# Optimization experiments

Hardware: AMD Instinct MI355X
Metric: run time of the kernel (lower is better)

Reference implementation:

```python
import jax, jax.numpy as jnp
import numpy as np
import math

T = 120      # frame_num == audio_len == max_seq_len
D = 64       # hidden_layer_size
H = 2        # n_head
DH = D // H
DFF = 2 * D
DOUT = 31
PERIOD = 10
EPS = 1e-5
NEG = -1e9
SCALE = 1.0 / math.sqrt(DH)
SLOPES = (1.0 / 16.0, 1.0 / 256.0)  # ALiBi slopes for n_head=2


def _pe():
    # PeriodicPositionalEncoding: sinusoid over one period, tiled
    pos = jnp.arange(PERIOD, dtype=jnp.float32)[:, None]
    div = jnp.exp(jnp.arange(0, D, 2, dtype=jnp.float32) * (-math.log(10000.0) / D))
    s, c = jnp.sin(pos * div), jnp.cos(pos * div)
    pe = jnp.stack([s, c], axis=-1).reshape(PERIOD, D)  # interleave sin/cos
    return jnp.tile(pe, (T // PERIOD + 1, 1))[:T]


def _alibi_mask():
    # causal mask + ALiBi bias: alibi[i,j] = -slope * floor((i-j)/period) for j<=i
    slopes = jnp.array(SLOPES, dtype=jnp.float32)
    i = jnp.arange(T)[:, None]
    j = jnp.arange(T)[None, :]
    rel = ((i - j) // PERIOD).astype(jnp.float32)
    return jnp.where(j <= i, -slopes[:, None, None] * rel, NEG)  # [H,T,T]


def _ln(x, g, b):
    m = x.mean(-1, keepdims=True)
    v = ((x - m) ** 2).mean(-1, keepdims=True)
    return (x - m) / jnp.sqrt(v + EPS) * g + b


def setup_inputs() -> dict:
    key = jax.random.key(0)
    ks = iter(jax.random.split(key, 32))
    n = lambda shape, s=0.05: jax.random.normal(next(ks), shape, dtype=jnp.float32) * s
    inp = {
        'audio': jax.random.normal(next(ks), (1, T, 1024), dtype=jnp.float32),
        'W_audio': n((D, 1024)), 'b_audio': n((D,)),
        'obj_W': n((D, 5)),
        'Wq': n((D, D)), 'bq': n((D,)), 'Wk': n((D, D)), 'bk': n((D,)),
        'Wv': n((D, D)), 'bv': n((D,)), 'Wo': n((D, D)), 'bo': n((D,)),
        'Wv2': n((D, D)), 'bv2': n((D,)), 'Wo2': n((D, D)), 'bo2': n((D,)),
        'g1': jnp.ones((D,)), 'be1': jnp.zeros((D,)),
        'g2': jnp.ones((D,)), 'be2': jnp.zeros((D,)),
        'g3': jnp.ones((D,)), 'be3': jnp.zeros((D,)),
        'W1': n((DFF, D)), 'c1': n((DFF,)), 'W2': n((D, DFF)), 'c2': n((D,)),
        'Wr': n((DOUT, D)), 'br': n((DOUT,)), 'Wm': n((D, DOUT)), 'bm': n((D,)),
    }
    return inp


def _forward(audio, W_audio, b_audio, obj_W, Wq, bq, Wk, bk, Wv, bv, Wo, bo,
             Wv2, bv2, Wo2, bo2, g1, be1, g2, be2, g3, be3,
             W1, c1, W2, c2, Wr, br, Wm, bm):
    mem = audio[0] @ W_audio.T + b_audio          # [S,D], S == T
    style = obj_W[:, 0]                            # obj_vector @ [1,0,0,0,0]
    pe = _pe()
    mask = _alibi_mask()
    slopes = jnp.array(SLOPES, dtype=jnp.float32)
    jarr = jnp.arange(T)

    # enc_dec_mask leaves exactly one memory key per target row (anti-diagonal
    # from the end); the feedback row t at step t always attends memory[-1],
    # so its cross-attn output is just the projected value of the last frame.
    cross_last = (mem[-1] @ Wv2.T + bv2) @ Wo2.T + bo2  # [D]

    def step(emb, t):
        # decode only the last row (row t) of the growing sequence; 1-layer
        # post-norm decoder => row t depends only on input rows 0..t.
        x = emb + pe                                 # PPE over prefix
        xq = jnp.take(x, t, axis=0)                  # [D]
        q = (xq @ Wq.T + bq).reshape(H, DH)
        k = (x @ Wk.T + bk).reshape(T, H, DH)
        v = (x @ Wv.T + bv).reshape(T, H, DH)
        bias = jnp.where(jarr <= t,
                         -slopes[:, None] * ((t - jarr) // PERIOD).astype(jnp.float32),
                         NEG)                        # [H,T]
        sc = jnp.einsum('hd,shd->hs', q, k) * SCALE + bias
        a = jax.nn.softmax(sc, axis=-1)
        sa = jnp.einsum('hs,shd->hd', a, v).reshape(D) @ Wo.T + bo
        h1 = _ln(xq + sa, g1, be1)
        h2 = _ln(h1 + cross_last, g2, be2)
        h3 = _ln(h2 + jax.nn.relu(h2 @ W1.T + c1) @ W2.T + c2, g3, be3)
        new = (h3 @ Wr.T + br) @ Wm.T + bm + style   # vertice_map(vertice_map_r(.)) + style
        emb = jax.lax.dynamic_update_slice(emb, new[None, :], (t + 1, 0))
        return emb, None

    emb0 = jnp.zeros((T, D), audio.dtype).at[0].set(style)
    emb, _ = jax.lax.scan(step, emb0, jnp.arange(T - 1))

    # final full-length decode (last loop iteration of the torch module)
    x = emb + pe
    q = (x @ Wq.T + bq).reshape(T, H, DH)
    k = (x @ Wk.T + bk).reshape(T, H, DH)
    v = (x @ Wv.T + bv).reshape(T, H, DH)
    sc = jnp.einsum('thd,shd->hts', q, k) * SCALE + mask
    a = jax.nn.softmax(sc, axis=-1)
    sa = jnp.einsum('hts,shd->thd', a, v).reshape(T, D) @ Wo.T + bo
    h1 = _ln(x + sa, g1, be1)
    # at length T with S == T the enc_dec_mask aligns target row j <-> memory row j
    cross = (mem @ Wv2.T + bv2) @ Wo2.T + bo2
    h2 = _ln(h1 + cross, g2, be2)
    h3 = _ln(h2 + jax.nn.relu(h2 @ W1.T + c1) @ W2.T + c2, g3, be3)
    return (h3 @ Wr.T + br)[None]                    # [1,T,31]


def reference(audio, W_audio, b_audio, obj_W, Wq, bq, Wk, bk, Wv, bv, Wo, bo,
              Wv2, bv2, Wo2, bo2, g1, be1, g2, be2, g3, be3,
              W1, c1, W2, c2, Wr, br, Wm, bm):
    return _forward(audio, W_audio, b_audio, obj_W, Wq, bq, Wk, bk, Wv, bv, Wo, bo,
                    Wv2, bv2, Wo2, bo2, g1, be1, g2, be2, g3, be3,
                    W1, c1, W2, c2, Wr, br, Wm, bm)
```

## Files before the change

kernel.cpp:

```cpp
#include <hip/hip_runtime.h>

typedef unsigned short u16;
typedef unsigned int   u32;
typedef _Float16 f16;
typedef f16 h2 __attribute__((ext_vector_type(2)));
typedef f16 h4 __attribute__((ext_vector_type(4)));
typedef f16 h8 __attribute__((ext_vector_type(8)));

#define T_    120
#define D_    64
#define DOUT_ 31
#define KROW_ 68
#define VROW_ 132

#if defined(__has_builtin)
#if __has_builtin(__builtin_amdgcn_fdot2)
#define DOT2(a,b,c) __builtin_amdgcn_fdot2((a),(b),(c),false)
#endif
#endif
#ifndef DOT2
#define DOT2(a,b,c) ((float)(a).x*(float)(b).x + ((float)(a).y*(float)(b).y + (c)))
#endif
#define SHV(x,i,j) __builtin_shufflevector((x),(x),(i),(j))

__device__ __forceinline__ h2 pk(float a, float b){
#if defined(__has_builtin) && __has_builtin(__builtin_amdgcn_cvt_pkrtz)
  return __builtin_bit_cast(h2, __builtin_amdgcn_cvt_pkrtz(a, b));
#else
  h2 r; r.x = (f16)a; r.y = (f16)b; return r;
#endif
}
__device__ __forceinline__ float b2f(u16 u){ return __uint_as_float(((u32)u) << 16); }
__device__ __forceinline__ float2 bp2(u32 u){
  float2 r; r.x = __uint_as_float(u << 16); r.y = __uint_as_float(u & 0xffff0000u); return r;
}
__device__ __forceinline__ u16 f2bu(float f){
  u32 u = __float_as_uint(f);
  u32 r = u + 0x7fffu + ((u >> 16) & 1u);
  return (u16)(r >> 16);
}
__device__ __forceinline__ u16 f2h16(float x){
  f16 v = (f16)x; u16 r; __builtin_memcpy(&r, &v, 2); return r;
}
__device__ __forceinline__ float fast_rcp(float x){
#if defined(__has_builtin) && __has_builtin(__builtin_amdgcn_rcpf)
  return __builtin_amdgcn_rcpf(x);
#else
  return 1.f / x;
#endif
}
#define WSYNC() do{ __asm__ __volatile__("" ::: "memory"); __builtin_amdgcn_wave_barrier(); }while(0)

__device__ __forceinline__ float dpp_sum(float x){
  int t;
  t = __builtin_amdgcn_update_dpp(0, __float_as_int(x), 0x111, 0xf, 0xf, true); x += __int_as_float(t);
  t = __builtin_amdgcn_update_dpp(0, __float_as_int(x), 0x112, 0xf, 0xf, true); x += __int_as_float(t);
  t = __builtin_amdgcn_update_dpp(0, __float_as_int(x), 0x114, 0xf, 0xf, true); x += __int_as_float(t);
  t = __builtin_amdgcn_update_dpp(0, __float_as_int(x), 0x118, 0xf, 0xf, true); x += __int_as_float(t);
  t = __builtin_amdgcn_update_dpp(0, __float_as_int(x), 0x142, 0xf, 0xf, true); x += __int_as_float(t);
  t = __builtin_amdgcn_update_dpp(0, __float_as_int(x), 0x143, 0xf, 0xf, true); x += __int_as_float(t);
  return __int_as_float(__builtin_amdgcn_readlane(__float_as_int(x), 63));
}
__device__ __forceinline__ float dpp_max_pos(float x){
  int t;
  t = __builtin_amdgcn_update_dpp(0, __float_as_int(x), 0x111, 0xf, 0xf, true); x = fmaxf(x, __int_as_float(t));
  t = __builtin_amdgcn_update_dpp(0, __float_as_int(x), 0x112, 0xf, 0xf, true); x = fmaxf(x, __int_as_float(t));
  t = __builtin_amdgcn_update_dpp(0, __float_as_int(x), 0x114, 0xf, 0xf, true); x = fmaxf(x, __int_as_float(t));
  t = __builtin_amdgcn_update_dpp(0, __float_as_int(x), 0x118, 0xf, 0xf, true); x = fmaxf(x, __int_as_float(t));
  t = __builtin_amdgcn_update_dpp(0, __float_as_int(x), 0x142, 0xf, 0xf, true); x = fmaxf(x, __int_as_float(t));
  t = __builtin_amdgcn_update_dpp(0, __float_as_int(x), 0x143, 0xf, 0xf, true); x = fmaxf(x, __int_as_float(t));
  return __int_as_float(__builtin_amdgcn_readlane(__float_as_int(x), 63));
}
__device__ __forceinline__ float pe_val(int row, int i){
  const float coef = -0.28782313662425574f;
  int p = row % 10;
  float dv  = __expf((float)(i >> 1) * coef);
  float ang = (float)p * dv;
  return (i & 1) ? __cosf(ang) : __sinf(ang);
}
__device__ __forceinline__ void loadrow32(h2* dst, const float* row){
  #pragma unroll
  for (int r = 0; r < 16; ++r){
    float4 f = ((const float4*)row)[r];
    dst[2*r]   = pk(f.x, f.y);
    dst[2*r+1] = pk(f.z, f.w);
  }
}

__global__ __launch_bounds__(256) void k_pre(const float* __restrict__ audio,
                                             const float* __restrict__ Wa, const float* __restrict__ ba,
                                             const float* __restrict__ Wv2, const float* __restrict__ bv2,
                                             const float* __restrict__ Wo2, const float* __restrict__ bo2,
                                             const float* __restrict__ Wo, const float* __restrict__ W1,
                                             const float* __restrict__ W2, const float* __restrict__ Wr,
                                             const float* __restrict__ Wm, const float* __restrict__ br,
                                             const float* __restrict__ bm,
                                             float* __restrict__ cross, float* __restrict__ Ms,
                                             float* __restrict__ bMv,
                                             u16* __restrict__ wob, u16* __restrict__ w1b,
                                             u16* __restrict__ w2b, u16* __restrict__ wrb){
  const int b = blockIdx.x, tid = threadIdx.x;
  if (b == 120){
    for (int i = tid; i < 4096; i += 256) wob[i] = f2bu(Wo[i]);
    for (int i = tid; i < 8192; i += 256){ w1b[i] = f2bu(W1[i]); w2b[i] = f2bu(W2[i]); }
    for (int i = tid; i < 1984; i += 256) wrb[i] = f2bu(Wr[i]);
    for (int idx = tid; idx < 4096; idx += 256){
      int d = idx >> 6, e = idx & 63;
      float acc = 0.f;
      #pragma unroll
      for (int j = 0; j < 31; ++j) acc += Wm[d*31 + j] * Wr[j*64 + e];
      Ms[idx] = acc;
    }
    if (tid < 64){
      float acc = bm[tid];
      #pragma unroll
      for (int j = 0; j < 31; ++j) acc += Wm[tid*31 + j] * br[j];
      bMv[tid] = acc;
    }
    return;
  }
  __shared__ float ash[1024];
  __shared__ float msh[64], tsh[64];
  for (int i = tid; i < 1024; i += 256) ash[i] = audio[b*1024 + i];
  __syncthreads();
  const int w = tid >> 6, lane = tid & 63;
  for (int d = w*16; d < w*16 + 16; ++d){
    const float4* row = (const float4*)(Wa + d*1024);
    float acc = 0.f;
    #pragma unroll
    for (int m = 0; m < 4; ++m){
      float4 wp = row[lane + 64*m];
      int j = 4*(lane + 64*m);
      acc += wp.x*ash[j] + wp.y*ash[j+1] + wp.z*ash[j+2] + wp.w*ash[j+3];
    }
    acc = dpp_sum(acc);
    if (lane == 0) msh[d] = acc + ba[d];
  }
  __syncthreads();
  if (tid < 64){
    const float4* r1 = (const float4*)(Wv2 + tid*64);
    float a = bv2[tid];
    #pragma unroll
    for (int j = 0; j < 16; ++j){ float4 p = r1[j]; a += p.x*msh[4*j] + p.y*msh[4*j+1] + p.z*msh[4*j+2] + p.w*msh[4*j+3]; }
    tsh[tid] = a;
  }
  __syncthreads();
  if (tid < 64){
    const float4* r2 = (const float4*)(Wo2 + tid*64);
    float c = bo2[tid];
    #pragma unroll
    for (int j = 0; j < 16; ++j){ float4 p = r2[j]; c += p.x*tsh[4*j] + p.y*tsh[4*j+1] + p.z*tsh[4*j+2] + p.w*tsh[4*j+3]; }
    cross[b*64 + tid] = c;
  }
}

__global__ __launch_bounds__(128, 1) void k_scan(
    const float* __restrict__ objW,
    const float* __restrict__ Wq, const float* __restrict__ bq,
    const float* __restrict__ Wk, const float* __restrict__ bk,
    const float* __restrict__ Wv, const float* __restrict__ bv,
    const float* __restrict__ Wo, const float* __restrict__ bo,
    const float* __restrict__ g1, const float* __restrict__ be1,
    const float* __restrict__ g2, const float* __restrict__ be2,
    const float* __restrict__ g3, const float* __restrict__ be3,
    const float* __restrict__ W1, const float* __restrict__ c1,
    const float* __restrict__ W2, const float* __restrict__ c2,
    const float* __restrict__ Ms, const float* __restrict__ bMv,
    const float* __restrict__ cross,
    u16* __restrict__ xw16, u16* __restrict__ Kw16, u16* __restrict__ Vw16)
{
  __shared__ __align__(16) f16 KcS[128*KROW_];
  __shared__ __align__(16) f16 VcS[D_*VROW_];
  __shared__ __align__(16) f16 xwS[T_*D_];
  __shared__ __align__(16) f16 sch[256];
  __shared__ __align__(16) f16 xh[64], qh[64], h2h[64], h3h[64];
  __shared__ __align__(16) f16 at0h[64], at1h[64];
  __shared__ __align__(16) f16 fsh[128];
  __shared__ float h2f[64], xf[64];
  __shared__ float invSh;
  __shared__ float pe_tab[640];

  const int tid = threadIdx.x;
  const int i = tid & 63;
  const bool w0 = tid < 64;

  h2 A[32], B[32], C[32], D[32], E[32];
  float biasA=0.f, biasB=0.f, bo_r=0.f, c1r=0.f, c2_r=0.f, cls_r=0.f;
  float g1r=0.f,b1r=0.f,g2r=0.f,b2r=0.f;
  float mg_r=0.f, u_r=0.f;

  if (w0){
    loadrow32(A, Wq + i*64);
    loadrow32(B, Wv + i*64);
    loadrow32(C, Wo + i*64);
    loadrow32(D, W1 + i*64);
    biasA = bq[i]; biasB = bv[i]; bo_r = bo[i]; c1r = c1[i];
    g1r = g1[i]; b1r = be1[i]; g2r = g2[i]; b2r = be2[i];
    cls_r = cross[119*64 + i];
  } else {
    loadrow32(A, Wk + i*64);
    loadrow32(B, W1 + (64+i)*64);
    loadrow32(C, W2 + i*128);
    loadrow32(D, W2 + i*128 + 64);
    {
      const float4* mr  = (const float4*)(Ms + i*64);
      const float4* gv  = (const float4*)g3;
      const float4* b3v = (const float4*)be3;
      float mg = 0.f, mb = 0.f;
      #pragma unroll
      for (int r = 0; r < 16; ++r){
        float4 f = mr[r], g = gv[r], b = b3v[r];
        float e0 = f.x*g.x, e1 = f.y*g.y, e2 = f.z*g.z, e3 = f.w*g.w;
        E[2*r]   = pk(e0, e1);
        E[2*r+1] = pk(e2, e3);
        mg += (e0+e1)+(e2+e3);
        mb += f.x*b.x + f.y*b.y + f.z*b.z + f.w*b.w;
      }
      mg_r = mg;
      u_r  = bMv[i] + objW[i*5] + mb;
    }
    biasA = bk[i]; c1r = c1[64+i]; c2_r = c2[i];
  }
  { u32* p = (u32*)KcS; for (int idx = tid; idx < 128*KROW_/2; idx += 128) p[idx] = 0; }
  { u32* p = (u32*)VcS; for (int idx = tid; idx < D_*VROW_/2;  idx += 128) p[idx] = 0; }
  for (int idx = tid; idx < 640; idx += 128) pe_tab[idx] = pe_val(idx >> 6, idx & 63);
  if (w0){
    float st = objW[i*5];
    float x0 = st + pe_val(0, i);
    xf[i] = x0; xh[i] = (f16)x0; xwS[i] = (f16)x0;
  }
  __syncthreads();

  int pp = 1;
  for (int t = 0; t < T_-1; ++t){
    float e0r, e1r, inv0v;
    h8 xr[8];
    {
      const h8* xv = (const h8*)xh;
      #pragma unroll
      for (int r = 0; r < 8; ++r) xr[r] = xv[r];
      float a0=biasA,a1=0.f,a2=0.f,a3=0.f;
      #pragma unroll
      for (int r = 0; r < 8; ++r){
        h8 x = xr[r];
        a0 = DOT2(A[4*r+0], SHV(x,0,1), a0);
        a1 = DOT2(A[4*r+1], SHV(x,2,3), a1);
        a2 = DOT2(A[4*r+2], SHV(x,4,5), a2);
        a3 = DOT2(A[4*r+3], SHV(x,6,7), a3);
      }
      float qk = (a0+a1)+(a2+a3);
      if (w0) qh[i] = (f16)qk; else KcS[t*KROW_ + i] = (f16)qk;
    }
    __syncthreads();
    {
      if (w0){
        float v0=biasB,v1=0.f,v2=0.f,v3=0.f;
        #pragma unroll
        for (int r = 0; r < 8; ++r){
          h8 x = xr[r];
          v0 = DOT2(B[4*r+0], SHV(x,0,1), v0); v1 = DOT2(B[4*r+1], SHV(x,2,3), v1);
          v2 = DOT2(B[4*r+2], SHV(x,4,5), v2); v3 = DOT2(B[4*r+3], SHV(x,6,7), v3);
        }
        VcS[i*VROW_ + t] = (f16)((v0+v1)+(v2+v3));
      }
      const int h = tid >> 6, j = i;
      const h8* qv = (const h8*)(qh + h*32);
      const h4* k0 = (const h4*)(KcS + j*KROW_ + h*32);
      const h4* k1 = (const h4*)(KcS + (j+64)*KROW_ + h*32);
      float d0a=0.f,d0b=0.f,d1a=0.f,d1b=0.f;
      #pragma unroll
      for (int r = 0; r < 4; ++r){
        h8 q = qv[r];
        h4 ka = k0[2*r], kb = k0[2*r+1], kc = k1[2*r], kd = k1[2*r+1];
        d0a = DOT2(SHV(ka,0,1), SHV(q,0,1), d0a);
        d0b = DOT2(SHV(ka,2,3), SHV(q,2,3), d0b);
        d0a = DOT2(SHV(kb,0,1), SHV(q,4,5), d0a);
        d0b = DOT2(SHV(kb,2,3), SHV(q,6,7), d0b);
        d1a = DOT2(SHV(kc,0,1), SHV(q,0,1), d1a);
        d1b = DOT2(SHV(kc,2,3), SHV(q,2,3), d1b);
        d1a = DOT2(SHV(kd,0,1), SHV(q,4,5), d1a);
        d1b = DOT2(SHV(kd,2,3), SHV(q,6,7), d1b);
      }
      float d0 = d0a + d0b, d1 = d1a + d1b;
      const float slope = h ? 0.00390625f : 0.0625f;
      int r0 = (t - j) / 10, r1 = (t - j - 64) / 10;
      float s0 = d0*0.17677669529663687f - slope*(float)r0;
      float s1 = d1*0.17677669529663687f - slope*(float)r1;
      e0r = (j      <= t) ? __expf(fminf(s0, 8.f)) : 0.f;
      e1r = (j + 64 <= t) ? __expf(fminf(s1, 8.f)) : 0.f;
      sch[h*128 + j]      = (f16)e0r;
      sch[h*128 + j + 64] = (f16)e1r;
    }
    __syncthreads();
    {
      float den = dpp_sum(e0r + e1r);
      float inv = fast_rcp(den);
      inv0v = inv;
      if (tid == 64) invSh = inv;
      if (w0 || t >= 64){
        const int hd = i >> 5;
        const h8* av = (const h8*)(sch + hd*128) + (w0 ? 0 : 8);
        const h4* vv = (const h4*)(VcS + i*VROW_) + (w0 ? 0 : 16);
        float p0=0.f,p1=0.f,p2=0.f,p3=0.f;
        #pragma unroll
        for (int r = 0; r < 8; ++r){
          h8 a = av[r];
          h4 va = vv[2*r], vb = vv[2*r+1];
          p0 = DOT2(SHV(va,0,1), SHV(a,0,1), p0);
          p1 = DOT2(SHV(va,2,3), SHV(a,2,3), p1);
          p2 = DOT2(SHV(vb,0,1), SHV(a,4,5), p2);
          p3 = DOT2(SHV(vb,2,3), SHV(a,6,7), p3);
        }
        float p = (p0+p1)+(p2+p3);
        if (w0) at0h[i] = (f16)p; else at1h[i] = (f16)p;
      }
    }
    __syncthreads();
    if (w0){
      float inv1v = invSh;
      float xfv = xf[i];
      float l0=0.f,l1=0.f,hh0=0.f,hh1=0.f;
      {
        const h8* a0v = (const h8*)at0h;
        #pragma unroll
        for (int r = 0; r < 4; ++r){
          h8 x = a0v[r];
          l0 = DOT2(C[4*r+0], SHV(x,0,1), l0); l1 = DOT2(C[4*r+1], SHV(x,2,3), l1);
          l0 = DOT2(C[4*r+2], SHV(x,4,5), l0); l1 = DOT2(C[4*r+3], SHV(x,6,7), l1);
        }
        #pragma unroll
        for (int r = 4; r < 8; ++r){
          h8 x = a0v[r];
          hh0 = DOT2(C[4*r+0], SHV(x,0,1), hh0); hh1 = DOT2(C[4*r+1], SHV(x,2,3), hh1);
          hh0 = DOT2(C[4*r+2], SHV(x,4,5), hh0); hh1 = DOT2(C[4*r+3], SHV(x,6,7), hh1);
        }
      }
      if (t >= 64){
        const h8* a1v = (const h8*)at1h;
        #pragma unroll
        for (int r = 0; r < 4; ++r){
          h8 x = a1v[r];
          l0 = DOT2(C[4*r+0], SHV(x,0,1), l0); l1 = DOT2(C[4*r+1], SHV(x,2,3), l1);
          l0 = DOT2(C[4*r+2], SHV(x,4,5), l0); l1 = DOT2(C[4*r+3], SHV(x,6,7), l1);
        }
        #pragma unroll
        for (int r = 4; r < 8; ++r){
          h8 x = a1v[r];
          hh0 = DOT2(C[4*r+0], SHV(x,0,1), hh0); hh1 = DOT2(C[4*r+1], SHV(x,2,3), hh1);
          hh0 = DOT2(C[4*r+2], SHV(x,4,5), hh0); hh1 = DOT2(C[4*r+3], SHV(x,6,7), hh1);
        }
      }
      float sa = bo_r + inv0v*(l0+l1) + inv1v*(hh0+hh1);
      float y = xfv + sa;
      float s = dpp_sum(y), s2 = dpp_sum(y*y);
      float m = s*(1.f/64.f), var = fmaxf(s2*(1.f/64.f) - m*m, 0.f);
      float h1 = (y - m)*rsqrtf(var + 1e-5f)*g1r + b1r;
      float z = h1 + cls_r;
      float sz = dpp_sum(z), sz2 = dpp_sum(z*z);
      float mz = sz*(1.f/64.f), vz = fmaxf(sz2*(1.f/64.f) - mz*mz, 0.f);
      float h2v = (z - mz)*rsqrtf(vz + 1e-5f)*g2r + b2r;
      h2h[i] = (f16)h2v;
      h2f[i] = h2v;
    }
    __syncthreads();
    {
      const h8* hv = (const h8*)h2h;
      float a0=c1r, a1=0.f, a2=0.f, a3=0.f;
      if (w0){
        #pragma unroll
        for (int r = 0; r < 8; ++r){
          h8 x = hv[r];
          a0 = DOT2(D[4*r+0], SHV(x,0,1), a0);
          a1 = DOT2(D[4*r+1], SHV(x,2,3), a1);
          a2 = DOT2(D[4*r+2], SHV(x,4,5), a2);
          a3 = DOT2(D[4*r+3], SHV(x,6,7), a3);
        }
      } else {
        #pragma unroll
        for (int r = 0; r < 8; ++r){
          h8 x = hv[r];
          a0 = DOT2(B[4*r+0], SHV(x,0,1), a0);
          a1 = DOT2(B[4*r+1], SHV(x,2,3), a1);
          a2 = DOT2(B[4*r+2], SHV(x,4,5), a2);
          a3 = DOT2(B[4*r+3], SHV(x,6,7), a3);
        }
      }
      fsh[tid] = (f16)fmaxf((a0+a1)+(a2+a3), 0.f);
    }
    __syncthreads();
    if (!w0){
      float pe_c  = pe_tab[pp*64 + i];
      float h2v_s = h2f[i];
      const h8* fv = (const h8*)fsh;
      float a0=c2_r, a1=0.f, a2=0.f, a3=0.f;
      #pragma unroll
      for (int r = 0; r < 8; ++r){
        h8 x = fv[r];
        a0 = DOT2(C[4*r+0], SHV(x,0,1), a0);
        a1 = DOT2(C[4*r+1], SHV(x,2,3), a1);
        a2 = DOT2(C[4*r+2], SHV(x,4,5), a2);
        a3 = DOT2(C[4*r+3], SHV(x,6,7), a3);
      }
      #pragma unroll
      for (int r = 0; r < 8; ++r){
        h8 x = fv[8+r];
        a0 = DOT2(D[4*r+0], SHV(x,0,1), a0);
        a1 = DOT2(D[4*r+1], SHV(x,2,3), a1);
        a2 = DOT2(D[4*r+2], SHV(x,4,5), a2);
        a3 = DOT2(D[4*r+3], SHV(x,6,7), a3);
      }
      float y3 = h2v_s + (a0+a1)+(a2+a3);
      h3h[i] = (f16)y3;
      WSYNC();
      const h8* hv3 = (const h8*)h3h;
      h8 yr[8];
      #pragma unroll
      for (int r = 0; r < 8; ++r) yr[r] = hv3[r];
      float s = dpp_sum(y3), s2 = dpp_sum(y3*y3);
      float m = s*(1.f/64.f), var = fmaxf(s2*(1.f/64.f) - m*m, 0.f);
      float invs = rsqrtf(var + 1e-5f);
      float m0=0.f, m1=0.f, m2=0.f, m3=0.f;
      #pragma unroll
      for (int r = 0; r < 8; ++r){
        h8 x = yr[r];
        m0 = DOT2(E[4*r+0], SHV(x,0,1), m0);
        m1 = DOT2(E[4*r+1], SHV(x,2,3), m1);
        m2 = DOT2(E[4*r+2], SHV(x,4,5), m2);
        m3 = DOT2(E[4*r+3], SHV(x,6,7), m3);
      }
      float xn = ((m0+m1)+(m2+m3))*invs + (u_r - m*invs*mg_r) + pe_c;
      xf[i] = xn;
      xh[i] = (f16)xn;
      xwS[(t+1)*64 + i] = (f16)xn;
    }
    __syncthreads();
    pp = (pp == 9) ? 0 : pp + 1;
  }
  {
    const h8* xv = (const h8*)xh;
    if (w0){
      float v0=biasB,v1=0.f,v2=0.f,v3=0.f;
      #pragma unroll
      for (int r = 0; r < 8; ++r){
        h8 x = xv[r];
        v0 = DOT2(B[4*r+0], SHV(x,0,1), v0);
        v1 = DOT2(B[4*r+1], SHV(x,2,3), v1);
        v2 = DOT2(B[4*r+2], SHV(x,4,5), v2);
        v3 = DOT2(B[4*r+3], SHV(x,6,7), v3);
      }
      Vw16[119*64 + i] = f2h16((v0+v1)+(v2+v3));
    } else {
      float k0=biasA,k1=0.f,k2=0.f,k3=0.f;
      #pragma unroll
      for (int r = 0; r < 8; ++r){
        h8 x = xv[r];
        k0 = DOT2(A[4*r+0], SHV(x,0,1), k0);
        k1 = DOT2(A[4*r+1], SHV(x,2,3), k1);
        k2 = DOT2(A[4*r+2], SHV(x,4,5), k2);
        k3 = DOT2(A[4*r+3], SHV(x,6,7), k3);
      }
      Kw16[119*64 + i] = f2h16((k0+k1)+(k2+k3));
    }
  }
  {
    const u16* kc = (const u16*)KcS;
    const u16* vc = (const u16*)VcS;
    for (int idx = tid; idx < 119*64; idx += 128){
      int t_ = idx >> 6, d = idx & 63;
      Kw16[idx] = kc[t_*KROW_ + d];
      Vw16[idx] = vc[d*VROW_ + t_];
    }
    const u32* xs32 = (const u32*)xwS;
    for (int idx = tid; idx < T_*D_/2; idx += 128) ((u32*)xw16)[idx] = xs32[idx];
  }
}

__global__ __launch_bounds__(128) void k_final(
    const float* __restrict__ Wq, const float* __restrict__ bq, const float* __restrict__ bo,
    const float* __restrict__ g1, const float* __restrict__ be1,
    const float* __restrict__ g2, const float* __restrict__ be2,
    const float* __restrict__ g3, const float* __restrict__ be3,
    const float* __restrict__ c1, const float* __restrict__ c2, const float* __restrict__ br,
    const u16* __restrict__ wo_b, const u16* __restrict__ w1_b,
    const u16* __restrict__ w2_b, const u16* __restrict__ wr_b,
    const float* __restrict__ cross, const u16* __restrict__ xw16,
    const u16* __restrict__ Kw16, const u16* __restrict__ Vw16,
    float* __restrict__ out)
{
  __shared__ float xs[64], qs[64], at[64], h2s[64], h3s[64], fs[128], sc[256];
  const int irow = blockIdx.x, tid = threadIdx.x;
  const f16* xp = (const f16*)xw16;
  const f16* kp = (const f16*)Kw16;
  const f16* vp = (const f16*)Vw16;
  if (tid < 64) xs[tid] = (float)xp[irow*64 + tid];
  __syncthreads();
  if (tid < 64){
    const float4* wr_ = (const float4*)(Wq + tid*64);
    float acc = bq[tid];
    #pragma unroll
    for (int j = 0; j < 16; ++j){ float4 w = wr_[j]; acc += w.x*xs[4*j] + w.y*xs[4*j+1] + w.z*xs[4*j+2] + w.w*xs[4*j+3]; }
    qs[tid] = acc;
  }
  __syncthreads();
  {
    const int h = tid >> 6, j = tid & 63;
    const float* qh_ = qs + h*32;
    float d0 = 0.f, d1 = 0.f;
    const h4* k0 = (const h4*)(kp + j*64 + h*32);
    #pragma unroll
    for (int w = 0; w < 8; ++w){
      h4 p = k0[w];
      d0 += (float)p.x*qh_[4*w] + (float)p.y*qh_[4*w+1] + (float)p.z*qh_[4*w+2] + (float)p.w*qh_[4*w+3];
    }
    if (j < 56){
      const h4* k1 = (const h4*)(kp + (j+64)*64 + h*32);
      #pragma unroll
      for (int w = 0; w < 8; ++w){
        h4 p = k1[w];
        d1 += (float)p.x*qh_[4*w] + (float)p.y*qh_[4*w+1] + (float)p.z*qh_[4*w+2] + (float)p.w*qh_[4*w+3];
      }
    }
    const float slope = h ? 0.00390625f : 0.0625f;
    float s0 = (j      <= irow) ? d0*0.17677669529663687f - slope*(float)((irow-j)/10)    : -1e30f;
    float s1 = (j + 64 <= irow) ? d1*0.17677669529663687f - slope*(float)((irow-j-64)/10) : -1e30f;
    float m = dpp_max_pos(fmaxf(s0, s1) + 16384.f) - 16384.f;
    float e0 = (j      <= irow) ? __expf(s0 - m) : 0.f;
    float e1 = (j + 64 <= irow) ? __expf(s1 - m) : 0.f;
    float inv = 1.f / dpp_sum(e0 + e1);
    sc[h*128 + j]      = e0*inv;
    sc[h*128 + j + 64] = e1*inv;
  }
  __syncthreads();
  if (tid < 64){
    const float* a = sc + (tid >> 5)*128;
    float a0=0.f,a1=0.f,a2=0.f,a3=0.f;
    #pragma unroll
    for (int jj = 0; jj < 30; ++jj){
      a0 += a[4*jj]   * (float)vp[(4*jj)*64   + tid];
      a1 += a[4*jj+1] * (float)vp[(4*jj+1)*64 + tid];
      a2 += a[4*jj+2] * (float)vp[(4*jj+2)*64 + tid];
      a3 += a[4*jj+3] * (float)vp[(4*jj+3)*64 + tid];
    }
    at[tid] = (a0+a1)+(a2+a3);
  }
  __syncthreads();
  if (tid < 64){
    const u32* orow = (const u32*)(wo_b + tid*64);
    float acc = bo[tid];
    #pragma unroll
    for (int w = 0; w < 32; ++w){ float2 p = bp2(orow[w]); acc += p.x*at[2*w] + p.y*at[2*w+1]; }
    float y = xs[tid] + acc;
    float s = dpp_sum(y), s2 = dpp_sum(y*y);
    float m = s*(1.f/64.f), var = fmaxf(s2*(1.f/64.f) - m*m, 0.f);
    float h1 = (y - m)*rsqrtf(var + 1e-5f)*g1[tid] + be1[tid];
    float z = h1 + cross[irow*64 + tid];
    float sz = dpp_sum(z), sz2 = dpp_sum(z*z);
    float mz = sz*(1.f/64.f), vz = fmaxf(sz2*(1.f/64.f) - mz*mz, 0.f);
    h2s[tid] = (z - mz)*rsqrtf(vz + 1e-5f)*g2[tid] + be2[tid];
  }
  __syncthreads();
  {
    const u32* w1r = (const u32*)(w1_b + tid*64);
    float acc = c1[tid];
    #pragma unroll
    for (int w = 0; w < 32; ++w){ float2 p = bp2(w1r[w]); acc += p.x*h2s[2*w] + p.y*h2s[2*w+1]; }
    fs[tid] = fmaxf(acc, 0.f);
  }
  __syncthreads();
  if (tid < 64){
    const u32* w2r = (const u32*)(w2_b + tid*128);
    float acc = c2[tid];
    #pragma unroll
    for (int w = 0; w < 64; ++w){ float2 p = bp2(w2r[w]); acc += p.x*fs[2*w] + p.y*fs[2*w+1]; }
    float y = h2s[tid] + acc;
    float s = dpp_sum(y), s2 = dpp_sum(y*y);
    float m = s*(1.f/64.f), var = fmaxf(s2*(1.f/64.f) - m*m, 0.f);
    h3s[tid] = (y - m)*rsqrtf(var + 1e-5f)*g3[tid] + be3[tid];
  }
  __syncthreads();
  if (tid < DOUT_){
    const u32* rr = (const u32*)(wr_b + tid*64);
    float acc = br[tid];
    #pragma unroll
    for (int w = 0; w < 32; ++w){ float2 p = bp2(rr[w]); acc += p.x*h3s[2*w] + p.y*h3s[2*w+1]; }
    out[irow*DOUT_ + tid] = acc;
  }
}

extern "C" void kernel_launch(void* const* d_in, const int* in_sizes, int n_in,
                              void* d_out, int out_size, void* d_ws, size_t ws_size,
                              hipStream_t stream){
  const float* audio=(const float*)d_in[0];
  const float* Wa   =(const float*)d_in[1];
  const float* ba   =(const float*)d_in[2];
  const float* objW =(const float*)d_in[3];
  const float* Wq   =(const float*)d_in[4];
  const float* bq   =(const float*)d_in[5];
  const float* Wk   =(const float*)d_in[6];
  const float* bk   =(const float*)d_in[7];
  const float* Wv   =(const float*)d_in[8];
  const float* bv   =(const float*)d_in[9];
  const float* Wo   =(const float*)d_in[10];
  const float* bo   =(const float*)d_in[11];
  const float* Wv2  =(const float*)d_in[12];
  const float* bv2  =(const float*)d_in[13];
  const float* Wo2  =(const float*)d_in[14];
  const float* bo2  =(const float*)d_in[15];
  const float* g1   =(const float*)d_in[16];
  const float* be1  =(const float*)d_in[17];
  const float* g2   =(const float*)d_in[18];
  const float* be2  =(const float*)d_in[19];
  const float* g3   =(const float*)d_in[20];
  const float* be3  =(const float*)d_in[21];
  const float* W1   =(const float*)d_in[22];
  const float* c1   =(const float*)d_in[23];
  const float* W2   =(const float*)d_in[24];
  const float* c2   =(const float*)d_in[25];
  const float* Wr   =(const float*)d_in[26];
  const float* br   =(const float*)d_in[27];
  const float* Wm   =(const float*)d_in[28];
  const float* bm   =(const float*)d_in[29];

  float* ws    = (float*)d_ws;
  float* cross = ws;
  float* Ms    = ws + 7680;
  float* bMv   = ws + 11776;
  u16* xw16 = (u16*)(ws + 11840);
  u16* Kw16 = xw16 + 7680;
  u16* Vw16 = Kw16 + 7680;
  u16* wo_b = Vw16 + 7680;
  u16* w1_b = wo_b + 4096;
  u16* w2_b = w1_b + 8192;
  u16* wr_b = w2_b + 8192;
  float* out = (float*)d_out;

  k_pre  <<<dim3(121), dim3(256), 0, stream>>>(audio, Wa, ba, Wv2, bv2, Wo2, bo2,
                                               Wo, W1, W2, Wr, Wm, br, bm,
                                               cross, Ms, bMv, wo_b, w1_b, w2_b, wr_b);
  k_scan <<<dim3(1),   dim3(128), 0, stream>>>(objW, Wq, bq, Wk, bk, Wv, bv, Wo, bo,
                                               g1, be1, g2, be2, g3, be3,
                                               W1, c1, W2, c2, Ms, bMv,
                                               cross, xw16, Kw16, Vw16);
  k_final<<<dim3(120), dim3(128), 0, stream>>>(Wq, bq, bo, g1, be1, g2, be2, g3, be3,
                                               c1, c2, br, wo_b, w1_b, w2_b, wr_b,
                                               cross, xw16, Kw16, Vw16, out);
}
```

Before: 376.2 us.

## Restructure per-step work across waves to replace block barriers with wave syncs

Each of the two waves now computes a per-head half of Q and K, so only that wave's own data is needed before scoring, and a wave-level sync replaces a block barrier there. Each wave also does its own output-projection partial for its attention half. The whole FFN (W1 lo/hi plus W2 with interleaved packed weights) moves into wave 1, which removes two more block barriers from the serial 119-step loop. The cost is more per-wave serial work and more registers (an extra 64-entry packed array), which may lower occupancy or cause spills.

```diff
diff --git a/kernel.cpp b/kernel.cpp
--- a/kernel.cpp
+++ b/kernel.cpp
@@ -175,33 +175,46 @@
   __shared__ __align__(16) f16 sch[256];
   __shared__ __align__(16) f16 xh[64], qh[64], h2h[64], h3h[64];
   __shared__ __align__(16) f16 at0h[64], at1h[64];
-  __shared__ __align__(16) f16 fsh[128];
-  __shared__ float h2f[64], xf[64];
+  __shared__ __align__(16) u32 fsh2[64];
+  __shared__ float sa0lo[64], sa0hi[64];
   __shared__ float invSh;
   __shared__ float pe_tab[640];
 
   const int tid = threadIdx.x;
   const int i = tid & 63;
+  const int hh = tid >> 6;
   const bool w0 = tid < 64;
 
-  h2 A[32], B[32], C[32], D[32], E[32];
-  float biasA=0.f, biasB=0.f, bo_r=0.f, c1r=0.f, c2_r=0.f, cls_r=0.f;
+  h2 A[32], B[32], C[32], D[32], E[32], G[64];
+  float biasA=0.f, biasB=0.f, bo_r=0.f, c1lo=0.f, c1hi=0.f, c2_r=0.f, cls_r=0.f;
   float g1r=0.f,b1r=0.f,g2r=0.f,b2r=0.f;
   float mg_r=0.f, u_r=0.f;
-
+  float x_r = 0.f;
+
+  {
+    const int qi = hh*32 + (i & 31);
+    if (i < 32){ loadrow32(A, Wq + qi*64); biasA = bq[qi]; }
+    else       { loadrow32(A, Wk + qi*64); biasA = bk[qi]; }
+    loadrow32(C, Wo + i*64);
+  }
   if (w0){
-    loadrow32(A, Wq + i*64);
     loadrow32(B, Wv + i*64);
-    loadrow32(C, Wo + i*64);
-    loadrow32(D, W1 + i*64);
-    biasA = bq[i]; biasB = bv[i]; bo_r = bo[i]; c1r = c1[i];
-    g1r = g1[i]; b1r = be1[i]; g2r = g2[i]; b2r = be2[i];
-    cls_r = cross[119*64 + i];
+    biasB = bv[i];
   } else {
-    loadrow32(A, Wk + i*64);
-    loadrow32(B, W1 + (64+i)*64);
-    loadrow32(C, W2 + i*128);
-    loadrow32(D, W2 + i*128 + 64);
+    loadrow32(B, W1 + i*64);
+    loadrow32(D, W1 + (64+i)*64);
+    {
+      const float4* lo4 = (const float4*)(W2 + i*128);
+      const float4* hi4 = (const float4*)(W2 + i*128 + 64);
+      #pragma unroll
+      for (int r = 0; r < 16; ++r){
+        float4 a = lo4[r], b = hi4[r];
+        G[4*r+0] = pk(a.x, b.x);
+        G[4*r+1] = pk(a.y, b.y);
+        G[4*r+2] = pk(a.z, b.z);
+        G[4*r+3] = pk(a.w, b.w);
+      }
+    }
     {
       const float4* mr  = (const float4*)(Ms + i*64);
       const float4* gv  = (const float4*)g3;
@@ -219,21 +232,22 @@
       mg_r = mg;
       u_r  = bMv[i] + objW[i*5] + mb;
     }
-    biasA = bk[i]; c1r = c1[64+i]; c2_r = c2[i];
+    bo_r = bo[i]; c1lo = c1[i]; c1hi = c1[64+i]; c2_r = c2[i];
+    g1r = g1[i]; b1r = be1[i]; g2r = g2[i]; b2r = be2[i];
+    cls_r = cross[119*64 + i];
   }
   { u32* p = (u32*)KcS; for (int idx = tid; idx < 128*KROW_/2; idx += 128) p[idx] = 0; }
   { u32* p = (u32*)VcS; for (int idx = tid; idx < D_*VROW_/2;  idx += 128) p[idx] = 0; }
   for (int idx = tid; idx < 640; idx += 128) pe_tab[idx] = pe_val(idx >> 6, idx & 63);
-  if (w0){
-    float st = objW[i*5];
-    float x0 = st + pe_val(0, i);
-    xf[i] = x0; xh[i] = (f16)x0; xwS[i] = (f16)x0;
+  if (!w0){
+    float x0 = objW[i*5] + pe_val(0, i);
+    x_r = x0; xh[i] = (f16)x0; xwS[i] = (f16)x0;
   }
   __syncthreads();
 
   int pp = 1;
   for (int t = 0; t < T_-1; ++t){
-    float e0r, e1r, inv0v;
+    float e0r, e1r, inv_w, lo_w = 0.f, hi_w = 0.f;
     h8 xr[8];
     {
       const h8* xv = (const h8*)xh;
@@ -249,9 +263,10 @@
         a3 = DOT2(A[4*r+3], SHV(x,6,7), a3);
       }
       float qk = (a0+a1)+(a2+a3);
-      if (w0) qh[i] = (f16)qk; else KcS[t*KROW_ + i] = (f16)qk;
-    }
-    __syncthreads();
+      f16* dst = (i < 32) ? (qh + hh*32 + i) : (KcS + t*KROW_ + hh*32 + (i - 32));
+      *dst = (f16)qk;
+    }
+    WSYNC();
     {
       if (w0){
         float v0=biasB,v1=0.f,v2=0.f,v3=0.f;
@@ -263,10 +278,10 @@
         }
         VcS[i*VROW_ + t] = (f16)((v0+v1)+(v2+v3));
       }
-      const int h = tid >> 6, j = i;
-      const h8* qv = (const h8*)(qh + h*32);
-      const h4* k0 = (const h4*)(KcS + j*KROW_ + h*32);
-      const h4* k1 = (const h4*)(KcS + (j+64)*KROW_ + h*32);
+      const int j = i;
+      const h8* qv = (const h8*)(qh + hh*32);
+      const h4* k0 = (const h4*)(KcS + j*KROW_ + hh*32);
+      const h4* k1 = (const h4*)(KcS + (j+64)*KROW_ + hh*32);
       float d0a=0.f,d0b=0.f,d1a=0.f,d1b=0.f;
       #pragma unroll
       for (int r = 0; r < 4; ++r){
@@ -282,21 +297,20 @@
         d1b = DOT2(SHV(kd,2,3), SHV(q,6,7), d1b);
       }
       float d0 = d0a + d0b, d1 = d1a + d1b;
-      const float slope = h ? 0.00390625f : 0.0625f;
+      const float slope = hh ? 0.00390625f : 0.0625f;
       int r0 = (t - j) / 10, r1 = (t - j - 64) / 10;
       float s0 = d0*0.17677669529663687f - slope*(float)r0;
       float s1 = d1*0.17677669529663687f - slope*(float)r1;
       e0r = (j      <= t) ? __expf(fminf(s0, 8.f)) : 0.f;
       e1r = (j + 64 <= t) ? __expf(fminf(s1, 8.f)) : 0.f;
-      sch[h*128 + j]      = (f16)e0r;
-      sch[h*128 + j + 64] = (f16)e1r;
+      sch[hh*128 + j]      = (f16)e0r;
+      sch[hh*128 + j + 64] = (f16)e1r;
     }
     __syncthreads();
     {
       float den = dpp_sum(e0r + e1r);
-      float inv = fast_rcp(den);
-      inv0v = inv;
-      if (tid == 64) invSh = inv;
+      inv_w = fast_rcp(den);
+      if (tid == 0) invSh = inv_w;
       if (w0 || t >= 64){
         const int hd = i >> 5;
         const h8* av = (const h8*)(sch + hd*128) + (w0 ? 0 : 8);
@@ -312,46 +326,34 @@
           p3 = DOT2(SHV(vb,2,3), SHV(a,6,7), p3);
         }
         float p = (p0+p1)+(p2+p3);
-        if (w0) at0h[i] = (f16)p; else at1h[i] = (f16)p;
-      }
-    }
-    __syncthreads();
-    if (w0){
-      float inv1v = invSh;
-      float xfv = xf[i];
-      float l0=0.f,l1=0.f,hh0=0.f,hh1=0.f;
-      {
-        const h8* a0v = (const h8*)at0h;
+        f16* ath = w0 ? at0h : at1h;
+        ath[i] = (f16)p;
+        WSYNC();
+        const h8* pv = (const h8*)ath;
+        float l0=0.f,l1=0.f,q0=0.f,q1=0.f;
         #pragma unroll
         for (int r = 0; r < 4; ++r){
-          h8 x = a0v[r];
+          h8 x = pv[r];
           l0 = DOT2(C[4*r+0], SHV(x,0,1), l0); l1 = DOT2(C[4*r+1], SHV(x,2,3), l1);
           l0 = DOT2(C[4*r+2], SHV(x,4,5), l0); l1 = DOT2(C[4*r+3], SHV(x,6,7), l1);
         }
         #pragma unroll
         for (int r = 4; r < 8; ++r){
-          h8 x = a0v[r];
-          hh0 = DOT2(C[4*r+0], SHV(x,0,1), hh0); hh1 = DOT2(C[4*r+1], SHV(x,2,3), hh1);
-          hh0 = DOT2(C[4*r+2], SHV(x,4,5), hh0); hh1 = DOT2(C[4*r+3], SHV(x,6,7), hh1);
+          h8 x = pv[r];
+          q0 = DOT2(C[4*r+0], SHV(x,0,1), q0); q1 = DOT2(C[4*r+1], SHV(x,2,3), q1);
+          q0 = DOT2(C[4*r+2], SHV(x,4,5), q0); q1 = DOT2(C[4*r+3], SHV(x,6,7), q1);
         }
-      }
-      if (t >= 64){
-        const h8* a1v = (const h8*)at1h;
-        #pragma unroll
-        for (int r = 0; r < 4; ++r){
-          h8 x = a1v[r];
-          l0 = DOT2(C[4*r+0], SHV(x,0,1), l0); l1 = DOT2(C[4*r+1], SHV(x,2,3), l1);
-          l0 = DOT2(C[4*r+2], SHV(x,4,5), l0); l1 = DOT2(C[4*r+3], SHV(x,6,7), l1);
-        }
-        #pragma unroll
-        for (int r = 4; r < 8; ++r){
-          h8 x = a1v[r];
-          hh0 = DOT2(C[4*r+0], SHV(x,0,1), hh0); hh1 = DOT2(C[4*r+1], SHV(x,2,3), hh1);
-          hh0 = DOT2(C[4*r+2], SHV(x,4,5), hh0); hh1 = DOT2(C[4*r+3], SHV(x,6,7), hh1);
-        }
-      }
-      float sa = bo_r + inv0v*(l0+l1) + inv1v*(hh0+hh1);
-      float y = xfv + sa;
+        lo_w = l0 + l1;  hi_w = q0 + q1;
+      }
+      if (w0){ sa0lo[i] = lo_w; sa0hi[i] = hi_w; }
+    }
+    __syncthreads();
+    if (!w0){
+      float lo0 = sa0lo[i], hi0 = sa0hi[i];
+      float inv0 = invSh;
+      float pe_c = pe_tab[pp*64 + i];
+      float sa = bo_r + inv0*(lo0 + lo_w) + inv_w*(hi0 + hi_w);
+      float y = x_r + sa;
       float s = dpp_sum(y), s2 = dpp_sum(y*y);
       float m = s*(1.f/64.f), var = fmaxf(s2*(1.f/64.f) - m*m, 0.f);
       float h1 = (y - m)*rsqrtf(var + 1e-5f)*g1r + b1r;
@@ -360,76 +362,62 @@
       float mz = sz*(1.f/64.f), vz = fmaxf(sz2*(1.f/64.f) - mz*mz, 0.f);
       float h2v = (z - mz)*rsqrtf(vz + 1e-5f)*g2r + b2r;
       h2h[i] = (f16)h2v;
-      h2f[i] = h2v;
-    }
-    __syncthreads();
-    {
-      const h8* hv = (const h8*)h2h;
-      float a0=c1r, a1=0.f, a2=0.f, a3=0.f;
-      if (w0){
+      WSYNC();
+      h8 hr[8];
+      {
+        const h8* hv = (const h8*)h2h;
         #pragma unroll
-        for (int r = 0; r < 8; ++r){
-          h8 x = hv[r];
-          a0 = DOT2(D[4*r+0], SHV(x,0,1), a0);
-          a1 = DOT2(D[4*r+1], SHV(x,2,3), a1);
-          a2 = DOT2(D[4*r+2], SHV(x,4,5), a2);
-          a3 = DOT2(D[4*r+3], SHV(x,6,7), a3);
-        }
-      } else {
-        #pragma unroll
-        for (int r = 0; r < 8; ++r){
-          h8 x = hv[r];
-          a0 = DOT2(B[4*r+0], SHV(x,0,1), a0);
-          a1 = DOT2(B[4*r+1], SHV(x,2,3), a1);
-          a2 = DOT2(B[4*r+2], SHV(x,4,5), a2);
-          a3 = DOT2(B[4*r+3], SHV(x,6,7), a3);
-        }
-      }
-      fsh[tid] = (f16)fmaxf((a0+a1)+(a2+a3), 0.f);
-    }
-    __syncthreads();
-    if (!w0){
-      float pe_c  = pe_tab[pp*64 + i];
-      float h2v_s = h2f[i];
-      const h8* fv = (const h8*)fsh;
-      float a0=c2_r, a1=0.f, a2=0.f, a3=0.f;
+        for (int r = 0; r < 8; ++r) hr[r] = hv[r];
+      }
+      float a0=c1lo, a1=0.f, a2=0.f, a3=0.f;
+      float b0=c1hi, b1=0.f, b2=0.f, b3=0.f;
       #pragma unroll
       for (int r = 0; r < 8; ++r){
+        h8 x = hr[r];
+        a0 = DOT2(B[4*r+0], SHV(x,0,1), a0);
+        a1 = DOT2(B[4*r+1], SHV(x,2,3), a1);
+        a2 = DOT2(B[4*r+2], SHV(x,4,5), a2);
+        a3 = DOT2(B[4*r+3], SHV(x,6,7), a3);
+        b0 = DOT2(D[4*r+0], SHV(x,0,1), b0);
+        b1 = DOT2(D[4*r+1], SHV(x,2,3), b1);
+        b2 = DOT2(D[4*r+2], SHV(x,4,5), b2);
+        b3 = DOT2(D[4*r+3], SHV(x,6,7), b3);
+      }
+      float fLo = fmaxf((a0+a1)+(a2+a3), 0.f);
+      float fHi = fmaxf((b0+b1)+(b2+b3), 0.f);
+      fsh2[i] = __builtin_bit_cast(u32, pk(fLo, fHi));
+      WSYNC();
+      const h8* fv = (const h8*)fsh2;
+      float f0=c2_r, f1=0.f, f2=0.f, f3=0.f;
+      #pragma unroll
+      for (int r = 0; r < 16; ++r){
         h8 x = fv[r];
-        a0 = DOT2(C[4*r+0], SHV(x,0,1), a0);
-        a1 = DOT2(C[4*r+1], SHV(x,2,3), a1);
-        a2 = DOT2(C[4*r+2], SHV(x,4,5), a2);
-        a3 = DOT2(C[4*r+3], SHV(x,6,7), a3);
-      }
-      #pragma unroll
-      for (int r = 0; r < 8; ++r){
-        h8 x = fv[8+r];
-        a0 = DOT2(D[4*r+0], SHV(x,0,1), a0);
-        a1 = DOT2(D[4*r+1], SHV(x,2,3), a1);
-        a2 = DOT2(D[4*r+2], SHV(x,4,5), a2);
-        a3 = DOT2(D[4*r+3], SHV(x,6,7), a3);
-      }
-      float y3 = h2v_s + (a0+a1)+(a2+a3);
+        f0 = DOT2(G[4*r+0], SHV(x,0,1), f0);
+        f1 = DOT2(G[4*r+1], SHV(x,2,3), f1);
+        f2 = DOT2(G[4*r+2], SHV(x,4,5), f2);
+        f3 = DOT2(G[4*r+3], SHV(x,6,7), f3);
+      }
+      float y3 = h2v + (f0+f1)+(f2+f3);
       h3h[i] = (f16)y3;
       WSYNC();
-      const h8* hv3 = (const h8*)h3h;
+      const h8* yv3 = (const h8*)h3h;
       h8 yr[8];
       #pragma unroll
-      for (int r = 0; r < 8; ++r) yr[r] = hv3[r];
-      float s = dpp_sum(y3), s2 = dpp_sum(y3*y3);
-      float m = s*(1.f/64.f), var = fmaxf(s2*(1.f/64.f) - m*m, 0.f);
-      float invs = rsqrtf(var + 1e-5f);
-      float m0=0.f, m1=0.f, m2=0.f, m3=0.f;
+      for (int r = 0; r < 8; ++r) yr[r] = yv3[r];
+      float s3 = dpp_sum(y3), s32 = dpp_sum(y3*y3);
+      float m3 = s3*(1.f/64.f), v3 = fmaxf(s32*(1.f/64.f) - m3*m3, 0.f);
+      float invs = rsqrtf(v3 + 1e-5f);
+      float m0=0.f, m1=0.f, m2=0.f, mm3=0.f;
       #pragma unroll
       for (int r = 0; r < 8; ++r){
         h8 x = yr[r];
         m0 = DOT2(E[4*r+0], SHV(x,0,1), m0);
         m1 = DOT2(E[4*r+1], SHV(x,2,3), m1);
         m2 = DOT2(E[4*r+2], SHV(x,4,5), m2);
-        m3 = DOT2(E[4*r+3], SHV(x,6,7), m3);
-      }
-      float xn = ((m0+m1)+(m2+m3))*invs + (u_r - m*invs*mg_r) + pe_c;
-      xf[i] = xn;
+        mm3 = DOT2(E[4*r+3], SHV(x,6,7), mm3);
+      }
+      float xn = ((m0+m1)+(m2+mm3))*invs + (u_r - m3*invs*mg_r) + pe_c;
+      x_r = xn;
       xh[i] = (f16)xn;
       xwS[(t+1)*64 + i] = (f16)xn;
     }
@@ -438,28 +426,32 @@
   }
   {
     const h8* xv = (const h8*)xh;
+    h8 xr[8];
+    #pragma unroll
+    for (int r = 0; r < 8; ++r) xr[r] = xv[r];
     if (w0){
       float v0=biasB,v1=0.f,v2=0.f,v3=0.f;
       #pragma unroll
       for (int r = 0; r < 8; ++r){
-        h8 x = xv[r];
+        h8 x = xr[r];
         v0 = DOT2(B[4*r+0], SHV(x,0,1), v0);
         v1 = DOT2(B[4*r+1], SHV(x,2,3), v1);
         v2 = DOT2(B[4*r+2], SHV(x,4,5), v2);
         v3 = DOT2(B[4*r+3], SHV(x,6,7), v3);
       }
       Vw16[119*64 + i] = f2h16((v0+v1)+(v2+v3));
-    } else {
+    }
+    if (i >= 32){
       float k0=biasA,k1=0.f,k2=0.f,k3=0.f;
       #pragma unroll
       for (int r = 0; r < 8; ++r){
-        h8 x = xv[r];
+        h8 x = xr[r];
         k0 = DOT2(A[4*r+0], SHV(x,0,1), k0);
         k1 = DOT2(A[4*r+1], SHV(x,2,3), k1);
         k2 = DOT2(A[4*r+2], SHV(x,4,5), k2);
         k3 = DOT2(A[4*r+3], SHV(x,6,7), k3);
       }
-      Kw16[119*64 + i] = f2h16((k0+k1)+(k2+k3));
+      Kw16[119*64 + hh*32 + (i-32)] = f2h16((k0+k1)+(k2+k3));
     }
   }
   {
```

Result: slower. 390.7 us (+3.9%).
